# Kernel optimization log

Hardware: AMD Instinct MI355X
Metric: run time of the kernel (lower is better)

The kernel has to match this reference:

```python
import jax, jax.numpy as jnp
import numpy as np

B, T, I, H, K = 32, 1024, 512, 512, 2


def _causal_conv1d(x_bit, w_hik, b_h):
    # x_bit: [B, I, T]; left-pad K-1 zeros (ConstantPad1d((K-1, 0)))
    xp = jnp.pad(x_bit, ((0, 0), (0, 0), (K - 1, 0)))
    y = jax.lax.conv_general_dilated(
        xp, w_hik, window_strides=(1,), padding='VALID',
        dimension_numbers=('NCH', 'OIH', 'NCH'))  # [B, H, T]
    return y + b_h[None, :, None]


def setup_inputs() -> dict:
    key = jax.random.key(0)
    k1, k2, k3 = jax.random.split(key, 3)
    bound = 1.0 / np.sqrt(I * K)  # torch Conv1d default init scale
    return {
        'inputs': jax.random.normal(k1, (B, T, I), dtype=jnp.float32),
        'init_state': jnp.zeros((B, H), dtype=jnp.float32),
        'Wz': jax.random.uniform(k2, (H, I, K), jnp.float32, -bound, bound),
        'bz': jnp.zeros((H,), dtype=jnp.float32),
        'Wf': jax.random.uniform(k3, (H, I, K), jnp.float32, -bound, bound),
        'bf': jnp.zeros((H,), dtype=jnp.float32),
    }


def reference(inputs, init_state, Wz, bz, Wf, bf):
    # init_state is accepted but unused in the original forward (mode='f').
    x = inputs.transpose(0, 2, 1)                      # [B, I, T]
    raw_f = _causal_conv1d(x, Wf, bf).transpose(0, 2, 1)  # [B, T, H]
    raw_z = _causal_conv1d(x, Wz, bz).transpose(0, 2, 1)  # [B, T, H]

    log_f = jax.nn.log_sigmoid(raw_f)
    log_one_minus_f = jax.nn.log_sigmoid(-raw_f)
    log_z = jax.nn.log_sigmoid(raw_z)

    # recurrent_gates[t] = sum_{s>t} log_f[s]  (suffix sum of log_f over time, excluding t=0 shift)
    rg = log_f[:, 1:, :]                               # [B, T-1, H]
    cs = jnp.cumsum(rg, axis=1)
    rg = rg - cs + cs[:, -1:, :]
    rg = jnp.concatenate([rg, jnp.zeros((inputs.shape[0], 1, rg.shape[2]), dtype=rg.dtype)], axis=1)  # [B, T, H]

    log_hidden = jax.lax.cumlogsumexp(log_z + log_one_minus_f + rg, axis=1)
    hidden = jnp.exp(log_hidden - rg)
    return hidden
```

## Files before the change

kernel.cpp:

```cpp
#include <hip/hip_runtime.h>
#include <hip/hip_bf16.h>
#include <cstddef>
#include <cstdint>

#define B_  32
#define T_  1024
#define I_  512
#define H_  512
#define M_  (B_ * T_)
#define TP_ 1025

typedef __bf16 bf16x8  __attribute__((ext_vector_type(8)));
typedef float  floatx4 __attribute__((ext_vector_type(4)));
typedef unsigned short ushort8v __attribute__((ext_vector_type(8)));
typedef unsigned long long u64;

__device__ __forceinline__ unsigned short f2bf(float f) {
    uint32_t u = __float_as_uint(f);
    return (unsigned short)((u + 0x7FFFu + ((u >> 16) & 1u)) >> 16);
}
__device__ __forceinline__ float sigm(float x) {
    return __builtin_amdgcn_rcpf(1.f + __expf(-x));
}

#define GLL(src, dst) __builtin_amdgcn_global_load_lds( \
    (const __attribute__((address_space(1))) void*)(src), \
    (__attribute__((address_space(3))) void*)(dst), 16, 0, 0)

#define NB_BUILD 8200
#define NB_PACK  512
#define NB_ZERO  256

__global__ __launch_bounds__(256) void prep(const float* __restrict__ x,
                                            const float* __restrict__ Wf,
                                            const float* __restrict__ Wz,
                                            unsigned short* __restrict__ Ab2,
                                            unsigned short* __restrict__ Wq,
                                            uint4* __restrict__ HpubZ,
                                            uint32_t* __restrict__ cnt) {
    if (blockIdx.x < NB_BUILD) {
        int g = blockIdx.x * 256 + threadIdx.x;
        int idx8 = g << 3;
        int row = idx8 >> 9;
        int col = idx8 & 511;
        int b    = (int)((unsigned)row / TP_);
        int trow = row - b * TP_;
        ushort8v o = {0, 0, 0, 0, 0, 0, 0, 0};
        if (trow > 0) {
            const float* src = &x[((size_t)b * T_ + (trow - 1)) * I_ + col];
            float4 v0 = *(const float4*)src;
            float4 v1 = *(const float4*)(src + 4);
            o[0] = f2bf(v0.x); o[1] = f2bf(v0.y); o[2] = f2bf(v0.z); o[3] = f2bf(v0.w);
            o[4] = f2bf(v1.x); o[5] = f2bf(v1.y); o[6] = f2bf(v1.z); o[7] = f2bf(v1.w);
        }
        *(ushort8v*)&Ab2[(size_t)idx8] = o;
    } else if (blockIdx.x < NB_BUILD + NB_PACK) {
        int cid = (blockIdx.x - NB_BUILD) * 256 + threadIdx.x;
        int lane = cid & 63;
        int c    = (cid >> 6) & 3;
        int wn   = (cid >> 8) & 1;
        int ksub = (cid >> 9) & 31;
        int ni   = (cid >> 14) & 3;
        int gate = (cid >> 16) & 1;
        int n_col = ni * 128 + wn * 64 + c * 16 + (lane & 15);
        const float* G = gate ? Wz : Wf;
        ushort8v o;
        #pragma unroll
        for (int j = 0; j < 8; ++j) {
            int k   = ksub * 32 + (lane >> 4) * 8 + j;
            int tap = k >> 9;
            int i   = k & 511;
            o[j] = f2bf(G[n_col * (I_ * 2) + i * 2 + tap]);
        }
        *(ushort8v*)&Wq[(size_t)cid * 8] = o;
    } else {
        int g = (blockIdx.x - NB_BUILD - NB_PACK) * 256 + threadIdx.x;
        HpubZ[g] = make_uint4(0, 0, 0, 0);
        if (g == 0) *cnt = 0;
    }
}

__global__ __launch_bounds__(256, 2) void mfma_gemm_scan(
        const unsigned short* __restrict__ Ab2,
        const unsigned short* __restrict__ Wq,
        const float* __restrict__ biasF,
        const float* __restrict__ biasZ,
        float* __restrict__ out,
        u64* __restrict__ Hpub,
        uint32_t* __restrict__ counter) {
    __shared__ unsigned short smem[36864];
    __shared__ uint32_t vid_s;

    const int tid = threadIdx.x;
    if (tid == 0) vid_s = atomicAdd(counter, 1u);
    __syncthreads();
    const int vid   = (int)vid_s;
    const int low3  = vid & 7;
    const int ni    = (vid >> 3) & 3;
    const int rem   = vid >> 5;
    const int pos   = rem >> 2;
    const int b     = ((rem & 3) << 3) | low3;
    const int chain = ni * 32 + b;
    const int h0    = ni * 128;
    const int browBase = b * TP_ + pos * 128;

    const int lane = tid & 63;
    const int wave = tid >> 6;
    const int wm   = wave >> 1, wn = wave & 1;
    const int lm   = lane & 15, quad = lane >> 4;

    const int c0 = wave * 128 + lane;
    const int c1 = c0 + 64;
    const int r0 = c0 >> 2, q0 = (c0 & 3) ^ ((r0 >> 2) & 3);
    const int r1 = c1 >> 2, q1 = (c1 & 3) ^ ((r1 >> 2) & 3);

    const unsigned short* pA0 = Ab2 + (size_t)(browBase + r0) * 512 + q0 * 8;
    const unsigned short* pA1 = Ab2 + (size_t)(browBase + r1) * 512 + q1 * 8;

    const unsigned short* pB = Wq + (size_t)(wave >> 1) * 524288
                                  + ni * 131072 + (wave & 1) * 2048 + lane * 8;

    int offA[4];
    #pragma unroll
    for (int r = 0; r < 4; ++r) {
        int ml = wm * 64 + r * 16 + lm;
        offA[r] = (4 * ml + (quad ^ ((ml >> 2) & 3))) * 8;
    }
    const int offBF = wn * 4 * 512 + lane * 8;
    const int offBZ = (8 + wn * 4) * 512 + lane * 8;

    floatx4 accF[4][4] = {};
    floatx4 accZ[4][4] = {};

#define ISSUE(ksub, sA, sB) do {                                        \
        const int aoff_ = (((ksub) >> 4) * 512) + (((ksub) & 15) * 32); \
        GLL(pA0 + aoff_, (sA) + wave * 1024);                           \
        GLL(pA1 + aoff_, (sA) + wave * 1024 + 512);                     \
        const unsigned short* bs_ = pB + (ksub) * 4096;                 \
        unsigned short* bd_ = (sB) + wave * 4 * 512;                    \
        GLL(bs_,        bd_);                                           \
        GLL(bs_ + 512,  bd_ + 512);                                     \
        GLL(bs_ + 1024, bd_ + 1024);                                    \
        GLL(bs_ + 1536, bd_ + 1536);                                    \
    } while (0)

#define COMPUTE(sA, sB) do {                                            \
        bf16x8 af_[4], bF_[4], bZ_[4];                                  \
        _Pragma("unroll")                                               \
        for (int c = 0; c < 4; ++c) {                                   \
            bF_[c] = *(const bf16x8*)((sB) + offBF + c * 512);          \
            bZ_[c] = *(const bf16x8*)((sB) + offBZ + c * 512);          \
        }                                                               \
        _Pragma("unroll")                                               \
        for (int r = 0; r < 4; ++r)                                     \
            af_[r] = *(const bf16x8*)((sA) + offA[r]);                  \
        __builtin_amdgcn_s_setprio(1);                                  \
        _Pragma("unroll")                                               \
        for (int r = 0; r < 4; ++r) {                                   \
            _Pragma("unroll")                                           \
            for (int c = 0; c < 4; ++c) {                               \
                accF[r][c] = __builtin_amdgcn_mfma_f32_16x16x32_bf16(   \
                                af_[r], bF_[c], accF[r][c], 0, 0, 0);   \
                accZ[r][c] = __builtin_amdgcn_mfma_f32_16x16x32_bf16(   \
                                af_[r], bZ_[c], accZ[r][c], 0, 0, 0);   \
            }                                                           \
        }                                                               \
        __builtin_amdgcn_s_setprio(0);                                  \
    } while (0)

    unsigned short* s0 = smem;
    unsigned short* s1 = smem + 12288;
    unsigned short* s2 = smem + 24576;

    ISSUE(0, s0, s0 + 4096);
    ISSUE(1, s1, s1 + 4096);

    for (int k = 0; k < 30; ++k) {
        asm volatile("s_waitcnt vmcnt(6)");
        __builtin_amdgcn_s_barrier();
        asm volatile("" ::: "memory");
        ISSUE(k + 2, s2, s2 + 4096);
        COMPUTE(s0, s0 + 4096);
        unsigned short* t_ = s0; s0 = s1; s1 = s2; s2 = t_;
    }
    asm volatile("s_waitcnt vmcnt(6)");
    __builtin_amdgcn_s_barrier();
    asm volatile("" ::: "memory");
    COMPUTE(s0, s0 + 4096);
    { unsigned short* t_ = s0; s0 = s1; s1 = s2; s2 = t_; }
    asm volatile("s_waitcnt vmcnt(0)");
    __builtin_amdgcn_s_barrier();
    asm volatile("" ::: "memory");
    COMPUTE(s0, s0 + 4096);
#undef ISSUE
#undef COMPUTE
    __syncthreads();

    float bfv[4], bzv[4];
    #pragma unroll
    for (int c = 0; c < 4; ++c) {
        int hc = h0 + wn * 64 + c * 16 + lm;
        bfv[c] = biasF[hc];
        bzv[c] = biasZ[hc];
    }

    float2* seg  = (float2*)smem;
    float*  hinL = (float*)&smem[16384];

    #pragma unroll
    for (int r = 0; r < 4; ++r) {
        const int sid = wm * 16 + r * 4 + quad;
        #pragma unroll
        for (int c = 0; c < 4; ++c) {
            float A = 1.f, C = 0.f;
            #pragma unroll
            for (int v = 0; v < 4; ++v) {
                float f = sigm(accF[r][c][v] + bfv[c]);
                float z = sigm(accZ[r][c][v] + bzv[c]);
                accF[r][c][v] = f;
                accZ[r][c][v] = z;
                A *= f;
                C = fmaf(f, C - z, z);
            }
            seg[sid * 128 + wn * 64 + c * 16 + lm] = make_float2(A, C);
        }
    }
    __syncthreads();

    float Hin = 0.f;
    if (tid < 128) {
        float At = 1.f, Ct = 0.f;
        #pragma unroll 8
        for (int s = 0; s < 32; ++s) {
            float2 sc = seg[s * 128 + tid];
            Ct = fmaf(sc.x, Ct, sc.y);
            At *= sc.x;
        }
        if (pos > 0) {
            u64* p = &Hpub[((size_t)(pos - 1) * 128 + chain) * 128 + tid];
            u64 v;
            while (((v = atomicAdd(p, 0ull)) >> 32) == 0ull)
                __builtin_amdgcn_s_sleep(2);
            Hin = __uint_as_float((uint32_t)v);
        }
        if (pos < 7) {
            float Hout = fmaf(At, Hin, Ct);
            u64 pv = 0x100000000ull | (u64)__float_as_uint(Hout);
            atomicExch(&Hpub[((size_t)pos * 128 + chain) * 128 + tid], pv);
        }
        float run = Hin;
        #pragma unroll 8
        for (int s = 0; s < 32; ++s) {
            hinL[s * 128 + tid] = run;
            float2 sc = seg[s * 128 + tid];
            run = fmaf(sc.x, run, sc.y);
        }
    }
    __syncthreads();

    const int rowBase = b * T_ + pos * 128;
    #pragma unroll
    for (int r = 0; r < 4; ++r) {
        const int sid = wm * 16 + r * 4 + quad;
        #pragma unroll
        for (int c = 0; c < 4; ++c) {
            const int hc = h0 + wn * 64 + c * 16 + lm;
            float hs = hinL[sid * 128 + (hc - h0)];
            #pragma unroll
            for (int v = 0; v < 4; ++v) {
                float f = accF[r][c][v];
                float z = accZ[r][c][v];
                hs = fmaf(f, hs - z, z);
                const size_t row = (size_t)(rowBase + wm * 64 + r * 16 + quad * 4 + v);
                out[row * H_ + hc] = hs;
            }
        }
    }
}

extern "C" void kernel_launch(void* const* d_in, const int* in_sizes, int n_in,
                              void* d_out, int out_size, void* d_ws, size_t ws_size,
                              hipStream_t stream) {
    const float* x  = (const float*)d_in[0];
    const float* Wz = (const float*)d_in[2];
    const float* bz = (const float*)d_in[3];
    const float* bf = (const float*)d_in[5];
    const float* Wf = (const float*)d_in[4];
    float* out = (float*)d_out;

    char* ws = (char*)d_ws;
    unsigned short* Ab2  = (unsigned short*)(ws);
    unsigned short* Wq   = (unsigned short*)(ws + (size_t)34 * 1024 * 1024);
    u64*            Hpub = (u64*)(ws + (size_t)36 * 1024 * 1024);
    uint32_t*       cnt  = (uint32_t*)(ws + (size_t)37 * 1024 * 1024);

    prep<<<NB_BUILD + NB_PACK + NB_ZERO, 256, 0, stream>>>(
        x, Wf, Wz, Ab2, Wq, (uint4*)Hpub, cnt);

    mfma_gemm_scan<<<1024, 256, 0, stream>>>(Ab2, Wq, bf, bz, out, Hpub, cnt);
}
```

Before: 203.5 us.

## Halve N tile to 64 hidden units per block for three-block occupancy

Each block now covers 64 hidden columns instead of 128, which halves accumulator registers and shared memory. The launch bound rises to three blocks per CU and the grid doubles to 2048, with the chain indexing and Hpub layout remapped to 256 groups per position. The aim is more resident waves to hide load latency and to shorten the cross-block scan wait. In exchange, each A tile is loaded twice as often, arithmetic intensity per block drops, and there are twice as many inter-block handoff chains.

```diff
diff --git a/kernel.cpp b/kernel.cpp
--- a/kernel.cpp
+++ b/kernel.cpp
@@ -80,7 +80,7 @@
     }
 }
 
-__global__ __launch_bounds__(256, 2) void mfma_gemm_scan(
+__global__ __launch_bounds__(256, 3) void mfma_gemm_scan(
         const unsigned short* __restrict__ Ab2,
         const unsigned short* __restrict__ Wq,
         const float* __restrict__ biasF,
@@ -88,37 +88,37 @@
         float* __restrict__ out,
         u64* __restrict__ Hpub,
         uint32_t* __restrict__ counter) {
-    __shared__ unsigned short smem[36864];
+    __shared__ unsigned short smem[24576];
     __shared__ uint32_t vid_s;
 
     const int tid = threadIdx.x;
     if (tid == 0) vid_s = atomicAdd(counter, 1u);
     __syncthreads();
-    const int vid   = (int)vid_s;
-    const int low3  = vid & 7;
-    const int ni    = (vid >> 3) & 3;
-    const int rem   = vid >> 5;
-    const int pos   = rem >> 2;
-    const int b     = ((rem & 3) << 3) | low3;
-    const int chain = ni * 32 + b;
-    const int h0    = ni * 128;
+    const int vid  = (int)vid_s;
+    const int pos  = vid >> 8;
+    const int g    = vid & 255;
+    const int b    = (((g >> 6) & 3) << 3) | (g & 7);
+    const int nh   = (g >> 3) & 7;
+    const int h0   = nh * 64;
     const int browBase = b * TP_ + pos * 128;
 
     const int lane = tid & 63;
     const int wave = tid >> 6;
-    const int wm   = wave >> 1, wn = wave & 1;
+    const int wm   = wave >> 1;
+    const int wh   = wave & 1;
     const int lm   = lane & 15, quad = lane >> 4;
 
     const int c0 = wave * 128 + lane;
     const int c1 = c0 + 64;
     const int r0 = c0 >> 2, q0 = (c0 & 3) ^ ((r0 >> 2) & 3);
     const int r1 = c1 >> 2, q1 = (c1 & 3) ^ ((r1 >> 2) & 3);
-
     const unsigned short* pA0 = Ab2 + (size_t)(browBase + r0) * 512 + q0 * 8;
     const unsigned short* pA1 = Ab2 + (size_t)(browBase + r1) * 512 + q1 * 8;
 
-    const unsigned short* pB = Wq + (size_t)(wave >> 1) * 524288
-                                  + ni * 131072 + (wave & 1) * 2048 + lane * 8;
+    const unsigned short* pB0 = Wq + (size_t)(wave >> 1) * 524288
+                                   + (size_t)(nh >> 1) * 131072
+                                   + (nh & 1) * 2048
+                                   + ((wave & 1) * 2) * 512 + lane * 8;
 
     int offA[4];
     #pragma unroll
@@ -126,39 +126,36 @@
         int ml = wm * 64 + r * 16 + lm;
         offA[r] = (4 * ml + (quad ^ ((ml >> 2) & 3))) * 8;
     }
-    const int offBF = wn * 4 * 512 + lane * 8;
-    const int offBZ = (8 + wn * 4) * 512 + lane * 8;
-
-    floatx4 accF[4][4] = {};
-    floatx4 accZ[4][4] = {};
-
-#define ISSUE(ksub, sA, sB) do {                                        \
+    const int offBF = 4096 + wh * 1024 + lane * 8;
+    const int offBZ = offBF + 2048;
+
+    floatx4 accF[4][2] = {};
+    floatx4 accZ[4][2] = {};
+
+#define ISSUE(ksub, slot) do {                                          \
         const int aoff_ = (((ksub) >> 4) * 512) + (((ksub) & 15) * 32); \
-        GLL(pA0 + aoff_, (sA) + wave * 1024);                           \
-        GLL(pA1 + aoff_, (sA) + wave * 1024 + 512);                     \
-        const unsigned short* bs_ = pB + (ksub) * 4096;                 \
-        unsigned short* bd_ = (sB) + wave * 4 * 512;                    \
-        GLL(bs_,        bd_);                                           \
-        GLL(bs_ + 512,  bd_ + 512);                                     \
-        GLL(bs_ + 1024, bd_ + 1024);                                    \
-        GLL(bs_ + 1536, bd_ + 1536);                                    \
+        GLL(pA0 + aoff_, (slot) + wave * 1024);                         \
+        GLL(pA1 + aoff_, (slot) + wave * 1024 + 512);                   \
+        const unsigned short* bs_ = pB0 + (ksub) * 4096;                \
+        GLL(bs_,       (slot) + 4096 + wave * 1024);                    \
+        GLL(bs_ + 512, (slot) + 4096 + wave * 1024 + 512);              \
     } while (0)
 
-#define COMPUTE(sA, sB) do {                                            \
-        bf16x8 af_[4], bF_[4], bZ_[4];                                  \
-        _Pragma("unroll")                                               \
-        for (int c = 0; c < 4; ++c) {                                   \
-            bF_[c] = *(const bf16x8*)((sB) + offBF + c * 512);          \
-            bZ_[c] = *(const bf16x8*)((sB) + offBZ + c * 512);          \
-        }                                                               \
+#define COMPUTE(slot) do {                                              \
+        bf16x8 af_[4], bF_[2], bZ_[2];                                  \
         _Pragma("unroll")                                               \
         for (int r = 0; r < 4; ++r)                                     \
-            af_[r] = *(const bf16x8*)((sA) + offA[r]);                  \
+            af_[r] = *(const bf16x8*)((slot) + offA[r]);                \
+        _Pragma("unroll")                                               \
+        for (int c = 0; c < 2; ++c) {                                   \
+            bF_[c] = *(const bf16x8*)((slot) + offBF + c * 512);        \
+            bZ_[c] = *(const bf16x8*)((slot) + offBZ + c * 512);        \
+        }                                                               \
         __builtin_amdgcn_s_setprio(1);                                  \
         _Pragma("unroll")                                               \
         for (int r = 0; r < 4; ++r) {                                   \
             _Pragma("unroll")                                           \
-            for (int c = 0; c < 4; ++c) {                               \
+            for (int c = 0; c < 2; ++c) {                               \
                 accF[r][c] = __builtin_amdgcn_mfma_f32_16x16x32_bf16(   \
                                 af_[r], bF_[c], accF[r][c], 0, 0, 0);   \
                 accZ[r][c] = __builtin_amdgcn_mfma_f32_16x16x32_bf16(   \
@@ -169,49 +166,49 @@
     } while (0)
 
     unsigned short* s0 = smem;
-    unsigned short* s1 = smem + 12288;
-    unsigned short* s2 = smem + 24576;
-
-    ISSUE(0, s0, s0 + 4096);
-    ISSUE(1, s1, s1 + 4096);
+    unsigned short* s1 = smem + 8192;
+    unsigned short* s2 = smem + 16384;
+
+    ISSUE(0, s0);
+    ISSUE(1, s1);
 
     for (int k = 0; k < 30; ++k) {
-        asm volatile("s_waitcnt vmcnt(6)");
+        asm volatile("s_waitcnt vmcnt(4)");
         __builtin_amdgcn_s_barrier();
         asm volatile("" ::: "memory");
-        ISSUE(k + 2, s2, s2 + 4096);
-        COMPUTE(s0, s0 + 4096);
+        ISSUE(k + 2, s2);
+        COMPUTE(s0);
         unsigned short* t_ = s0; s0 = s1; s1 = s2; s2 = t_;
     }
-    asm volatile("s_waitcnt vmcnt(6)");
+    asm volatile("s_waitcnt vmcnt(4)");
     __builtin_amdgcn_s_barrier();
     asm volatile("" ::: "memory");
-    COMPUTE(s0, s0 + 4096);
+    COMPUTE(s0);
     { unsigned short* t_ = s0; s0 = s1; s1 = s2; s2 = t_; }
     asm volatile("s_waitcnt vmcnt(0)");
     __builtin_amdgcn_s_barrier();
     asm volatile("" ::: "memory");
-    COMPUTE(s0, s0 + 4096);
+    COMPUTE(s0);
 #undef ISSUE
 #undef COMPUTE
     __syncthreads();
 
-    float bfv[4], bzv[4];
-    #pragma unroll
-    for (int c = 0; c < 4; ++c) {
-        int hc = h0 + wn * 64 + c * 16 + lm;
+    float bfv[2], bzv[2];
+    #pragma unroll
+    for (int c = 0; c < 2; ++c) {
+        int hc = h0 + wh * 32 + c * 16 + lm;
         bfv[c] = biasF[hc];
         bzv[c] = biasZ[hc];
     }
 
     float2* seg  = (float2*)smem;
-    float*  hinL = (float*)&smem[16384];
+    float*  hinL = (float*)&smem[8192];
 
     #pragma unroll
     for (int r = 0; r < 4; ++r) {
         const int sid = wm * 16 + r * 4 + quad;
         #pragma unroll
-        for (int c = 0; c < 4; ++c) {
+        for (int c = 0; c < 2; ++c) {
             float A = 1.f, C = 0.f;
             #pragma unroll
             for (int v = 0; v < 4; ++v) {
@@ -222,22 +219,23 @@
                 A *= f;
                 C = fmaf(f, C - z, z);
             }
-            seg[sid * 128 + wn * 64 + c * 16 + lm] = make_float2(A, C);
-        }
-    }
-    __syncthreads();
-
-    float Hin = 0.f;
-    if (tid < 128) {
+            seg[sid * 64 + wh * 32 + c * 16 + lm] = make_float2(A, C);
+        }
+    }
+    __syncthreads();
+
+    if (tid < 64) {
+        const int h = tid;
         float At = 1.f, Ct = 0.f;
         #pragma unroll 8
         for (int s = 0; s < 32; ++s) {
-            float2 sc = seg[s * 128 + tid];
+            float2 sc = seg[s * 64 + h];
             Ct = fmaf(sc.x, Ct, sc.y);
             At *= sc.x;
         }
+        float Hin = 0.f;
         if (pos > 0) {
-            u64* p = &Hpub[((size_t)(pos - 1) * 128 + chain) * 128 + tid];
+            u64* p = &Hpub[((size_t)(pos - 1) * 256 + g) * 64 + h];
             u64 v;
             while (((v = atomicAdd(p, 0ull)) >> 32) == 0ull)
                 __builtin_amdgcn_s_sleep(2);
@@ -246,13 +244,13 @@
         if (pos < 7) {
             float Hout = fmaf(At, Hin, Ct);
             u64 pv = 0x100000000ull | (u64)__float_as_uint(Hout);
-            atomicExch(&Hpub[((size_t)pos * 128 + chain) * 128 + tid], pv);
+            atomicExch(&Hpub[((size_t)pos * 256 + g) * 64 + h], pv);
         }
         float run = Hin;
         #pragma unroll 8
         for (int s = 0; s < 32; ++s) {
-            hinL[s * 128 + tid] = run;
-            float2 sc = seg[s * 128 + tid];
+            hinL[s * 64 + h] = run;
+            float2 sc = seg[s * 64 + h];
             run = fmaf(sc.x, run, sc.y);
         }
     }
@@ -263,16 +261,16 @@
     for (int r = 0; r < 4; ++r) {
         const int sid = wm * 16 + r * 4 + quad;
         #pragma unroll
-        for (int c = 0; c < 4; ++c) {
-            const int hc = h0 + wn * 64 + c * 16 + lm;
-            float hs = hinL[sid * 128 + (hc - h0)];
+        for (int c = 0; c < 2; ++c) {
+            const int hcl = wh * 32 + c * 16 + lm;
+            float hs = hinL[sid * 64 + hcl];
             #pragma unroll
             for (int v = 0; v < 4; ++v) {
                 float f = accF[r][c][v];
                 float z = accZ[r][c][v];
                 hs = fmaf(f, hs - z, z);
                 const size_t row = (size_t)(rowBase + wm * 64 + r * 16 + quad * 4 + v);
-                out[row * H_ + hc] = hs;
+                out[row * H_ + h0 + hcl] = hs;
             }
         }
     }
@@ -284,8 +282,8 @@
     const float* x  = (const float*)d_in[0];
     const float* Wz = (const float*)d_in[2];
     const float* bz = (const float*)d_in[3];
+    const float* Wf = (const float*)d_in[4];
     const float* bf = (const float*)d_in[5];
-    const float* Wf = (const float*)d_in[4];
     float* out = (float*)d_out;
 
     char* ws = (char*)d_ws;
@@ -297,5 +295,5 @@
     prep<<<NB_BUILD + NB_PACK + NB_ZERO, 256, 0, stream>>>(
         x, Wf, Wz, Ab2, Wq, (uint4*)Hpub, cnt);
 
-    mfma_gemm_scan<<<1024, 256, 0, stream>>>(Ab2, Wq, bf, bz, out, Hpub, cnt);
-}
+    mfma_gemm_scan<<<2048, 256, 0, stream>>>(Ab2, Wq, bf, bz, out, Hpub, cnt);
+}
```

New measurement: 216.3 us. +6.3%, slower.

## Load weight fragments directly to registers and use per-chain ticket counters

Applied to the files above, without the earlier changes.

The B (weight) tiles are now read straight from global memory into registers, double-buffered across k-steps, instead of being staged through LDS. Only the A tiles still go through LDS, which cuts shared memory from about 72KB to 48KB and removes LDS read traffic for B. The single global work counter is replaced by per-chain ticket counters, so each block derives its chain from its block index and takes a time position from its chain's ticket. The risk is more register pressure and exposed global-load latency for B, since each wave now fetches its own B fragments rather than sharing them through LDS.

```diff
diff --git a/kernel.cpp b/kernel.cpp
--- a/kernel.cpp
+++ b/kernel.cpp
@@ -37,7 +37,7 @@
                                             unsigned short* __restrict__ Ab2,
                                             unsigned short* __restrict__ Wq,
                                             uint4* __restrict__ HpubZ,
-                                            uint32_t* __restrict__ cnt) {
+                                            uint32_t* __restrict__ tickets) {
     if (blockIdx.x < NB_BUILD) {
         int g = blockIdx.x * 256 + threadIdx.x;
         int idx8 = g << 3;
@@ -76,7 +76,7 @@
     } else {
         int g = (blockIdx.x - NB_BUILD - NB_PACK) * 256 + threadIdx.x;
         HpubZ[g] = make_uint4(0, 0, 0, 0);
-        if (g == 0) *cnt = 0;
+        if (g < 128) tickets[g] = 0;
     }
 }
 
@@ -87,21 +87,21 @@
         const float* __restrict__ biasZ,
         float* __restrict__ out,
         u64* __restrict__ Hpub,
-        uint32_t* __restrict__ counter) {
-    __shared__ unsigned short smem[36864];
-    __shared__ uint32_t vid_s;
+        uint32_t* __restrict__ tickets) {
+    __shared__ unsigned short smem[24576];
+    __shared__ uint32_t pos_s;
 
     const int tid = threadIdx.x;
-    if (tid == 0) vid_s = atomicAdd(counter, 1u);
+    const int bid = blockIdx.x;
+    const int x   = bid & 7;
+    const int ni  = (bid >> 3) & 3;
+    const int q   = bid >> 5;
+    const int b   = ((q & 3) << 3) | x;
+    const int chain = ni * 32 + b;
+    if (tid == 0) pos_s = atomicAdd(&tickets[chain], 1u);
     __syncthreads();
-    const int vid   = (int)vid_s;
-    const int low3  = vid & 7;
-    const int ni    = (vid >> 3) & 3;
-    const int rem   = vid >> 5;
-    const int pos   = rem >> 2;
-    const int b     = ((rem & 3) << 3) | low3;
-    const int chain = ni * 32 + b;
-    const int h0    = ni * 128;
+    const int pos = (int)pos_s;
+    const int h0  = ni * 128;
     const int browBase = b * TP_ + pos * 128;
 
     const int lane = tid & 63;
@@ -117,8 +117,7 @@
     const unsigned short* pA0 = Ab2 + (size_t)(browBase + r0) * 512 + q0 * 8;
     const unsigned short* pA1 = Ab2 + (size_t)(browBase + r1) * 512 + q1 * 8;
 
-    const unsigned short* pB = Wq + (size_t)(wave >> 1) * 524288
-                                  + ni * 131072 + (wave & 1) * 2048 + lane * 8;
+    const unsigned short* pBF = Wq + ni * 131072 + wn * 2048 + lane * 8;
 
     int offA[4];
     #pragma unroll
@@ -126,74 +125,133 @@
         int ml = wm * 64 + r * 16 + lm;
         offA[r] = (4 * ml + (quad ^ ((ml >> 2) & 3))) * 8;
     }
-    const int offBF = wn * 4 * 512 + lane * 8;
-    const int offBZ = (8 + wn * 4) * 512 + lane * 8;
 
     floatx4 accF[4][4] = {};
     floatx4 accZ[4][4] = {};
-
-#define ISSUE(ksub, sA, sB) do {                                        \
+    bf16x8 bfA[4], bzA[4], bfB[4], bzB[4];
+
+#define ISSUE_A(ksub, sA) do {                                          \
         const int aoff_ = (((ksub) >> 4) * 512) + (((ksub) & 15) * 32); \
         GLL(pA0 + aoff_, (sA) + wave * 1024);                           \
         GLL(pA1 + aoff_, (sA) + wave * 1024 + 512);                     \
-        const unsigned short* bs_ = pB + (ksub) * 4096;                 \
-        unsigned short* bd_ = (sB) + wave * 4 * 512;                    \
-        GLL(bs_,        bd_);                                           \
-        GLL(bs_ + 512,  bd_ + 512);                                     \
-        GLL(bs_ + 1024, bd_ + 1024);                                    \
-        GLL(bs_ + 1536, bd_ + 1536);                                    \
     } while (0)
 
-#define COMPUTE(sA, sB) do {                                            \
-        bf16x8 af_[4], bF_[4], bZ_[4];                                  \
+#define LOADB(ksub, BF, BZ) do {                                        \
+        const unsigned short* pf_ = pBF + (ksub) * 4096;                \
         _Pragma("unroll")                                               \
         for (int c = 0; c < 4; ++c) {                                   \
-            bF_[c] = *(const bf16x8*)((sB) + offBF + c * 512);          \
-            bZ_[c] = *(const bf16x8*)((sB) + offBZ + c * 512);          \
+            BF[c] = *(const bf16x8*)(pf_ + c * 512);                    \
+            BZ[c] = *(const bf16x8*)(pf_ + 524288 + c * 512);           \
         }                                                               \
-        _Pragma("unroll")                                               \
-        for (int r = 0; r < 4; ++r)                                     \
-            af_[r] = *(const bf16x8*)((sA) + offA[r]);                  \
+    } while (0)
+
+#define MFMA32(AF, BF, BZ) do {                                         \
         __builtin_amdgcn_s_setprio(1);                                  \
         _Pragma("unroll")                                               \
         for (int r = 0; r < 4; ++r) {                                   \
             _Pragma("unroll")                                           \
             for (int c = 0; c < 4; ++c) {                               \
                 accF[r][c] = __builtin_amdgcn_mfma_f32_16x16x32_bf16(   \
-                                af_[r], bF_[c], accF[r][c], 0, 0, 0);   \
+                                AF[r], BF[c], accF[r][c], 0, 0, 0);     \
                 accZ[r][c] = __builtin_amdgcn_mfma_f32_16x16x32_bf16(   \
-                                af_[r], bZ_[c], accZ[r][c], 0, 0, 0);   \
+                                AF[r], BZ[c], accZ[r][c], 0, 0, 0);     \
             }                                                           \
         }                                                               \
         __builtin_amdgcn_s_setprio(0);                                  \
     } while (0)
 
+#define RDA(slot, AF) do {                                              \
+        _Pragma("unroll")                                               \
+        for (int r = 0; r < 4; ++r)                                     \
+            AF[r] = *(const bf16x8*)((slot) + offA[r]);                 \
+    } while (0)
+
+#define ROT() do { unsigned short* t_ = s0; s0 = s1; s1 = s2; s2 = t_; } while (0)
+
     unsigned short* s0 = smem;
-    unsigned short* s1 = smem + 12288;
-    unsigned short* s2 = smem + 24576;
-
-    ISSUE(0, s0, s0 + 4096);
-    ISSUE(1, s1, s1 + 4096);
-
-    for (int k = 0; k < 30; ++k) {
-        asm volatile("s_waitcnt vmcnt(6)");
+    unsigned short* s1 = smem + 4096;
+    unsigned short* s2 = smem + 8192;
+
+    ISSUE_A(0, s0);
+    ISSUE_A(1, s1);
+    LOADB(0, bfA, bzA);
+
+    {
+        asm volatile("s_waitcnt vmcnt(0)");
         __builtin_amdgcn_s_barrier();
         asm volatile("" ::: "memory");
-        ISSUE(k + 2, s2, s2 + 4096);
-        COMPUTE(s0, s0 + 4096);
-        unsigned short* t_ = s0; s0 = s1; s1 = s2; s2 = t_;
-    }
-    asm volatile("s_waitcnt vmcnt(6)");
-    __builtin_amdgcn_s_barrier();
-    asm volatile("" ::: "memory");
-    COMPUTE(s0, s0 + 4096);
-    { unsigned short* t_ = s0; s0 = s1; s1 = s2; s2 = t_; }
-    asm volatile("s_waitcnt vmcnt(0)");
-    __builtin_amdgcn_s_barrier();
-    asm volatile("" ::: "memory");
-    COMPUTE(s0, s0 + 4096);
-#undef ISSUE
-#undef COMPUTE
+        bf16x8 af_[4];
+        RDA(s0, af_);
+        LOADB(1, bfB, bzB);
+        ISSUE_A(2, s2);
+        __builtin_amdgcn_sched_barrier(0);
+        MFMA32(af_, bfA, bzA);
+        ROT();
+    }
+    for (int p = 0; p < 14; ++p) {
+        const int k1 = 2 * p + 1;
+        {
+            asm volatile("s_waitcnt vmcnt(2)");
+            __builtin_amdgcn_s_barrier();
+            asm volatile("" ::: "memory");
+            bf16x8 af_[4];
+            RDA(s0, af_);
+            LOADB(k1 + 1, bfA, bzA);
+            ISSUE_A(k1 + 2, s2);
+            __builtin_amdgcn_sched_barrier(0);
+            MFMA32(af_, bfB, bzB);
+            ROT();
+        }
+        {
+            asm volatile("s_waitcnt vmcnt(2)");
+            __builtin_amdgcn_s_barrier();
+            asm volatile("" ::: "memory");
+            bf16x8 af_[4];
+            RDA(s0, af_);
+            LOADB(k1 + 2, bfB, bzB);
+            ISSUE_A(k1 + 3, s2);
+            __builtin_amdgcn_sched_barrier(0);
+            MFMA32(af_, bfA, bzA);
+            ROT();
+        }
+    }
+    {
+        asm volatile("s_waitcnt vmcnt(2)");
+        __builtin_amdgcn_s_barrier();
+        asm volatile("" ::: "memory");
+        bf16x8 af_[4];
+        RDA(s0, af_);
+        LOADB(30, bfA, bzA);
+        ISSUE_A(31, s2);
+        __builtin_amdgcn_sched_barrier(0);
+        MFMA32(af_, bfB, bzB);
+        ROT();
+    }
+    {
+        asm volatile("s_waitcnt vmcnt(2)");
+        __builtin_amdgcn_s_barrier();
+        asm volatile("" ::: "memory");
+        bf16x8 af_[4];
+        RDA(s0, af_);
+        LOADB(31, bfB, bzB);
+        __builtin_amdgcn_sched_barrier(0);
+        MFMA32(af_, bfA, bzA);
+        ROT();
+    }
+    {
+        asm volatile("s_waitcnt vmcnt(0)");
+        __builtin_amdgcn_s_barrier();
+        asm volatile("" ::: "memory");
+        bf16x8 af_[4];
+        RDA(s0, af_);
+        __builtin_amdgcn_sched_barrier(0);
+        MFMA32(af_, bfB, bzB);
+    }
+#undef ISSUE_A
+#undef LOADB
+#undef MFMA32
+#undef RDA
+#undef ROT
     __syncthreads();
 
     float bfv[4], bzv[4];
@@ -227,7 +285,6 @@
     }
     __syncthreads();
 
-    float Hin = 0.f;
     if (tid < 128) {
         float At = 1.f, Ct = 0.f;
         #pragma unroll 8
@@ -236,6 +293,7 @@
             Ct = fmaf(sc.x, Ct, sc.y);
             At *= sc.x;
         }
+        float Hin = 0.f;
         if (pos > 0) {
             u64* p = &Hpub[((size_t)(pos - 1) * 128 + chain) * 128 + tid];
             u64 v;
@@ -284,18 +342,18 @@
     const float* x  = (const float*)d_in[0];
     const float* Wz = (const float*)d_in[2];
     const float* bz = (const float*)d_in[3];
+    const float* Wf = (const float*)d_in[4];
     const float* bf = (const float*)d_in[5];
-    const float* Wf = (const float*)d_in[4];
     float* out = (float*)d_out;
 
     char* ws = (char*)d_ws;
     unsigned short* Ab2  = (unsigned short*)(ws);
     unsigned short* Wq   = (unsigned short*)(ws + (size_t)34 * 1024 * 1024);
     u64*            Hpub = (u64*)(ws + (size_t)36 * 1024 * 1024);
-    uint32_t*       cnt  = (uint32_t*)(ws + (size_t)37 * 1024 * 1024);
+    uint32_t*       tkt  = (uint32_t*)(ws + (size_t)37 * 1024 * 1024);
 
     prep<<<NB_BUILD + NB_PACK + NB_ZERO, 256, 0, stream>>>(
-        x, Wf, Wz, Ab2, Wq, (uint4*)Hpub, cnt);
-
-    mfma_gemm_scan<<<1024, 256, 0, stream>>>(Ab2, Wq, bf, bz, out, Hpub, cnt);
-}
+        x, Wf, Wz, Ab2, Wq, (uint4*)Hpub, tkt);
+
+    mfma_gemm_scan<<<1024, 256, 0, stream>>>(Ab2, Wq, bf, bz, out, Hpub, tkt);
+}
```

Measured after the change: 193.4 us. 1.05x faster.
